# Optimization experiments

Hardware: AMD Instinct MI355X
Metric: run time of the kernel (lower is better)

The kernel has to match this reference:

```python
import jax, jax.numpy as jnp
import numpy as np

# dims
B, N, NF, NEF = 32, 256, 3, 3          # batch, nodes, node feats, edge feats
D, FF, H, L = 768, 3072, 12, 6         # embed, ffn, heads, layers
NA, ND, NE, NS = 512, 512, 512, 512    # vocab sizes (atoms, degrees, edges, spatial)
S = N + 1                              # +1 graph token
HD = D // H
SCALE = HD ** -0.5
EPS = 1e-5


def setup_inputs() -> dict:
    key = jax.random.key(0)
    ki = iter(jax.random.split(key, 64))
    def nrm(shape, std):
        return jax.random.normal(next(ki), shape, jnp.float32) * std
    lin_std = 0.02 / np.sqrt(L)
    inp = {}
    inp['x'] = jax.random.randint(next(ki), (B, N, NF), 0, NA)
    inp['attn_bias'] = jnp.zeros((B, S, S), jnp.float32)
    inp['spatial_pos'] = jax.random.randint(next(ki), (B, N, N), 0, NS)
    inp['attn_edge_type'] = jax.random.randint(next(ki), (B, N, N, NEF), 0, NE)
    inp['in_degree'] = jax.random.randint(next(ki), (B, N), 0, ND)
    inp['out_degree'] = jax.random.randint(next(ki), (B, N), 0, ND)
    # embedding tables (init_params overwrites padding rows with normals, so no zero row)
    inp['atom_emb'] = nrm((NA + 1, D), 0.02)
    inp['in_deg_emb'] = nrm((ND, D), 0.02)
    inp['out_deg_emb'] = nrm((ND, D), 0.02)
    inp['graph_token'] = nrm((1, D), 0.02)
    inp['spatial_emb'] = nrm((NS, H), 0.02)
    inp['edge_emb'] = nrm((NE + 1, H), 0.02)
    inp['virt_dist'] = nrm((1, H), 0.02)
    # stacked per-layer params (torch Linear convention: W is [out,in])
    for nm in ('Wq', 'Wk', 'Wv', 'Wo'):
        inp[nm] = nrm((L, D, D), lin_std)
    for nm in ('bq', 'bk', 'bv', 'bo'):
        inp[nm] = jnp.zeros((L, D), jnp.float32)
    inp['ln1_g'] = jnp.ones((L, D), jnp.float32); inp['ln1_b'] = jnp.zeros((L, D), jnp.float32)
    inp['ln2_g'] = jnp.ones((L, D), jnp.float32); inp['ln2_b'] = jnp.zeros((L, D), jnp.float32)
    inp['W1'] = nrm((L, FF, D), lin_std); inp['b1'] = jnp.zeros((L, FF), jnp.float32)
    inp['W2'] = nrm((L, D, FF), lin_std); inp['b2'] = jnp.zeros((L, D), jnp.float32)
    inp['fin_g'] = jnp.ones((D,), jnp.float32); inp['fin_b'] = jnp.zeros((D,), jnp.float32)
    return inp


def _ln(x, g, b):
    m = x.mean(-1, keepdims=True)
    v = jnp.mean((x - m) ** 2, axis=-1, keepdims=True)
    return (x - m) * jax.lax.rsqrt(v + EPS) * g + b


def _forward(x, attn_bias, spatial_pos, attn_edge_type, in_degree, out_degree, P):
    # --- GraphNodeFeature ---
    nf = P['atom_emb'][jnp.clip(x, 0, NA)].sum(-2)                     # [B,N,D]
    nf = nf + P['in_deg_emb'][jnp.clip(in_degree, 0, ND - 1)]
    nf = nf + P['out_deg_emb'][jnp.clip(out_degree, 0, ND - 1)]
    h = jnp.concatenate([jnp.broadcast_to(P['graph_token'][None], (B, 1, D)), nf], axis=1)  # [B,S,D]
    # --- GraphAttnBias ---
    inner = (P['spatial_emb'][jnp.clip(spatial_pos, 0, NS - 1)]
             + P['edge_emb'][jnp.clip(attn_edge_type, 0, NE)].mean(-2))  # [B,N,N,H]
    gb = jnp.broadcast_to(attn_bias[:, None], (B, H, S, S))
    gb = gb.at[:, :, 1:, 1:].add(jnp.transpose(inner, (0, 3, 1, 2)))
    t = P['virt_dist'].reshape(1, H, 1)
    gb = gb.at[:, :, 1:, 0].add(t)
    gb = gb.at[:, :, 0, :].add(t)
    # key padding mask: node is padded iff first feature index == 0; graph token never padded
    pad = jnp.concatenate([jnp.zeros((B, 1), bool), x[:, :, 0] == 0], axis=1)  # [B,S]
    maskk = pad[:, None, None, :]

    def step(hh, p):
        Wq, bq, Wk, bk, Wv, bv, Wo, bo, g1, bb_g1, W1, bf1, W2, bf2, g2, bb_g2 = p
        # pre-LN self-attention
        z = _ln(hh, g1, bb_g1)
        q = (jnp.einsum('bsi,oi->bso', z, Wq) + bq) * SCALE
        k = jnp.einsum('bsi,oi->bso', z, Wk) + bk
        v = jnp.einsum('bsi,oi->bso', z, Wv) + bv
        q = q.reshape(B, S, H, HD); k = k.reshape(B, S, H, HD); v = v.reshape(B, S, H, HD)
        scores = jnp.einsum('bqhd,bkhd->bhqk', q, k) + gb
        scores = jnp.where(maskk, -jnp.inf, scores)
        a = jax.nn.softmax(scores, axis=-1)
        o = jnp.einsum('bhqk,bkhd->bqhd', a, v).reshape(B, S, D)
        hh = hh + jnp.einsum('bsi,oi->bso', o, Wo) + bo
        # pre-LN FFN
        z = _ln(hh, g2, bb_g2)
        f = jax.nn.gelu(jnp.einsum('bsi,oi->bso', z, W1) + bf1, approximate=False)
        hh = hh + jnp.einsum('bsi,oi->bso', f, W2) + bf2
        return hh, None

    layer_params = (P['Wq'], P['bq'], P['Wk'], P['bk'], P['Wv'], P['bv'], P['Wo'], P['bo'],
                    P['ln1_g'], P['ln1_b'], P['W1'], P['b1'], P['W2'], P['b2'], P['ln2_g'], P['ln2_b'])
    h, _ = jax.lax.scan(step, h, layer_params)
    h = _ln(h, P['fin_g'], P['fin_b'])
    return h  # [B,S,D]


def reference(x, attn_bias, spatial_pos, attn_edge_type, in_degree, out_degree,
              atom_emb, in_deg_emb, out_deg_emb, graph_token, spatial_emb, edge_emb, virt_dist,
              Wq, Wk, Wv, Wo, bq, bk, bv, bo, ln1_g, ln1_b, ln2_g, ln2_b,
              W1, b1, W2, b2, fin_g, fin_b):
    P = dict(atom_emb=atom_emb, in_deg_emb=in_deg_emb, out_deg_emb=out_deg_emb,
             graph_token=graph_token, spatial_emb=spatial_emb, edge_emb=edge_emb, virt_dist=virt_dist,
             Wq=Wq, Wk=Wk, Wv=Wv, Wo=Wo, bq=bq, bk=bk, bv=bv, bo=bo,
             ln1_g=ln1_g, ln1_b=ln1_b, ln2_g=ln2_g, ln2_b=ln2_b,
             W1=W1, b1=b1, W2=W2, b2=b2, fin_g=fin_g, fin_b=fin_b)
    h = _forward(x, attn_bias, spatial_pos, attn_edge_type, in_degree, out_degree, P)
    node_rep = h[:, 1:, :]   # [B,N,D]
    graph_rep = h[:, 0, :]   # [B,D]
    return node_rep, graph_rep
```

## Files before the change

### kernel.cpp

```cpp
#include <hip/hip_runtime.h>
#include <hip/hip_bf16.h>
#include <math.h>

#define B_   32
#define N_   256
#define S_   257
#define D_   768
#define FF_  3072
#define H_   12
#define HD_  64
#define L_   6
#define NA_  512
#define ND_  512
#define NE_  512
#define NS_  512
#define SCALE_ 0.125f
#define EPS_ 1e-5f
#define NEG_BIG_ (-1e30f)

#define DD_  (D_ * D_)
#define FD_  (FF_ * D_)
#define WTOT_ (4 * DD_ + 2 * FD_)
#define QKVN_ 2304

typedef __hip_bfloat16 bf16;
typedef __attribute__((ext_vector_type(8))) short bf16x8;
typedef __attribute__((ext_vector_type(4))) float f32x4;

#define AS1 __attribute__((address_space(1)))
#define AS3 __attribute__((address_space(3)))

static __device__ __forceinline__ int iclamp(int v, int lo, int hi) {
    return v < lo ? lo : (v > hi ? hi : v);
}
static __device__ __forceinline__ float b2f(bf16 v) { return (float)v; }
static __device__ __forceinline__ short f2b(float f) {
    union { bf16 b; short s; } u; u.b = __float2bfloat16(f); return u.s;
}

__global__ __launch_bounds__(256) void embed_kernel(
    const int* __restrict__ x, const int* __restrict__ indeg,
    const int* __restrict__ outdeg, const float* __restrict__ atom_emb,
    const float* __restrict__ ine, const float* __restrict__ oute,
    const float* __restrict__ gtok, float* __restrict__ h)
{
    int row = blockIdx.x;
    int b = row / S_, s = row % S_;
    int t = threadIdx.x;
    float* hr = h + (size_t)row * D_;
    if (s == 0) {
        for (int d = t; d < D_; d += 256) hr[d] = gtok[d];
        return;
    }
    int n = s - 1;
    size_t xb = ((size_t)b * N_ + n) * 3;
    int i0 = iclamp(x[xb + 0], 0, NA_);
    int i1 = iclamp(x[xb + 1], 0, NA_);
    int i2 = iclamp(x[xb + 2], 0, NA_);
    int id = iclamp(indeg[(size_t)b * N_ + n], 0, ND_ - 1);
    int od = iclamp(outdeg[(size_t)b * N_ + n], 0, ND_ - 1);
    const float* a0 = atom_emb + (size_t)i0 * D_;
    const float* a1 = atom_emb + (size_t)i1 * D_;
    const float* a2 = atom_emb + (size_t)i2 * D_;
    const float* pi = ine + (size_t)id * D_;
    const float* po = oute + (size_t)od * D_;
    for (int d = t; d < D_; d += 256)
        hr[d] = a0[d] + a1[d] + a2[d] + pi[d] + po[d];
}

__global__ __launch_bounds__(256) void bias_kernel(
    const int* __restrict__ x, const float* __restrict__ ab,
    const int* __restrict__ sp, const int* __restrict__ et,
    const float* __restrict__ spemb, const float* __restrict__ eemb,
    const float* __restrict__ virt, bf16* __restrict__ bias)
{
    int row = blockIdx.x;
    int b = row / S_, q = row % S_;
    for (int k = threadIdx.x; k < S_; k += 256) {
        float abv = ab[((size_t)b * S_ + q) * S_ + k];
        bool masked = (k >= 1) && (x[((size_t)b * N_ + (k - 1)) * 3] == 0);
        size_t out_base = (size_t)b * H_ * S_ * S_ + (size_t)q * S_ + k;
        if (masked) {
            #pragma unroll
            for (int hh = 0; hh < H_; hh++)
                bias[out_base + (size_t)hh * S_ * S_] = __float2bfloat16(NEG_BIG_);
        } else if (q == 0 || k == 0) {
            #pragma unroll
            for (int hh = 0; hh < H_; hh++)
                bias[out_base + (size_t)hh * S_ * S_] = __float2bfloat16(abv + virt[hh]);
        } else {
            int spv = iclamp(sp[((size_t)b * N_ + (q - 1)) * N_ + (k - 1)], 0, NS_ - 1);
            size_t eb = (((size_t)b * N_ + (q - 1)) * N_ + (k - 1)) * 3;
            int e0 = iclamp(et[eb + 0], 0, NE_);
            int e1 = iclamp(et[eb + 1], 0, NE_);
            int e2 = iclamp(et[eb + 2], 0, NE_);
            #pragma unroll
            for (int hh = 0; hh < H_; hh++) {
                float inner = spemb[spv * H_ + hh]
                    + (eemb[e0 * H_ + hh] + eemb[e1 * H_ + hh] + eemb[e2 * H_ + hh]) * (1.0f / 3.0f);
                bias[out_base + (size_t)hh * S_ * S_] = __float2bfloat16(abv + inner);
            }
        }
    }
}

__global__ __launch_bounds__(256) void cvt_w_kernel(
    const float* __restrict__ Wq, const float* __restrict__ Wk,
    const float* __restrict__ Wv, const float* __restrict__ Wo,
    const float* __restrict__ W1, const float* __restrict__ W2,
    int layer, bf16* __restrict__ dst)
{
    size_t i = ((size_t)blockIdx.x * 256 + threadIdx.x) * 8;
    if (i >= (size_t)WTOT_) return;
    const float* src;
    float sc = 1.f;
    if (i < (size_t)4 * DD_) {
        size_t r = i / DD_;
        const float* base = (r == 0) ? Wq : (r == 1) ? Wk : (r == 2) ? Wv : Wo;
        src = base + (size_t)layer * DD_ + (i - r * DD_);
        if (r == 0) sc = SCALE_;
    } else if (i < (size_t)4 * DD_ + FD_) {
        src = W1 + (size_t)layer * FD_ + (i - (size_t)4 * DD_);
    } else {
        src = W2 + (size_t)layer * FD_ + (i - (size_t)4 * DD_ - FD_);
    }
    float4 a = *(const float4*)src;
    float4 c = *(const float4*)(src + 4);
    *(bf16x8*)((short*)dst + i) =
        (bf16x8){f2b(a.x * sc), f2b(a.y * sc), f2b(a.z * sc), f2b(a.w * sc),
                 f2b(c.x * sc), f2b(c.y * sc), f2b(c.z * sc), f2b(c.w * sc)};
}

__global__ __launch_bounds__(256) void pack_bias_kernel(
    const float* __restrict__ bq, const float* __restrict__ bk,
    const float* __restrict__ bv, int layer, float* __restrict__ bqkv)
{
    int i = blockIdx.x * 256 + threadIdx.x;
    if (i >= QKVN_) return;
    float v;
    if (i < D_)            v = bq[layer * D_ + i] * SCALE_;
    else if (i < 2 * D_)   v = bk[layer * D_ + (i - D_)];
    else                   v = bv[layer * D_ + (i - 2 * D_)];
    bqkv[i] = v;
}

__global__ __launch_bounds__(256) void ln_kernel(
    const float* __restrict__ x, bf16* __restrict__ y,
    const float* __restrict__ g, const float* __restrict__ b)
{
    int row = blockIdx.x;
    int t = threadIdx.x;
    const float* xr = x + (size_t)row * D_;
    bf16* yr = y + (size_t)row * D_;
    float v0 = xr[t], v1 = xr[t + 256], v2 = xr[t + 512];
    __shared__ float rs[256], rq[256];
    rs[t] = v0 + v1 + v2;
    rq[t] = v0 * v0 + v1 * v1 + v2 * v2;
    __syncthreads();
    for (int o = 128; o > 0; o >>= 1) {
        if (t < o) { rs[t] += rs[t + o]; rq[t] += rq[t + o]; }
        __syncthreads();
    }
    float mean = rs[0] * (1.0f / D_);
    float var = fmaxf(rq[0] * (1.0f / D_) - mean * mean, 0.f);
    float inv = rsqrtf(var + EPS_);
    yr[t]       = __float2bfloat16((v0 - mean) * inv * g[t]       + b[t]);
    yr[t + 256] = __float2bfloat16((v1 - mean) * inv * g[t + 256] + b[t + 256]);
    yr[t + 512] = __float2bfloat16((v2 - mean) * inv * g[t + 512] + b[t + 512]);
}

__global__ __launch_bounds__(256) void final_ln_kernel(
    const float* __restrict__ x, const float* __restrict__ g,
    const float* __restrict__ b, float* __restrict__ out)
{
    int row = blockIdx.x;
    int bb = row / S_, s = row % S_;
    int t = threadIdx.x;
    const float* xr = x + (size_t)row * D_;
    float v0 = xr[t], v1 = xr[t + 256], v2 = xr[t + 512];
    __shared__ float rs[256], rq[256];
    rs[t] = v0 + v1 + v2;
    rq[t] = v0 * v0 + v1 * v1 + v2 * v2;
    __syncthreads();
    for (int o = 128; o > 0; o >>= 1) {
        if (t < o) { rs[t] += rs[t + o]; rq[t] += rq[t + o]; }
        __syncthreads();
    }
    float mean = rs[0] * (1.0f / D_);
    float var = fmaxf(rq[0] * (1.0f / D_) - mean * mean, 0.f);
    float inv = rsqrtf(var + EPS_);
    float* dst = (s == 0) ? out + (size_t)B_ * N_ * D_ + (size_t)bb * D_
                          : out + ((size_t)bb * N_ + (s - 1)) * D_;
    dst[t]       = (v0 - mean) * inv * g[t]       + b[t];
    dst[t + 256] = (v1 - mean) * inv * g[t + 256] + b[t + 256];
    dst[t + 512] = (v2 - mean) * inv * g[t + 512] + b[t + 512];
}

template <typename TC, int MODE>
__global__ __launch_bounds__(256) void mgemm(
    const bf16* __restrict__ A, const bf16* __restrict__ W,
    const float* __restrict__ bias, const float* __restrict__ res,
    TC* __restrict__ C, int M, int N, int K, int gx)
{
    __shared__ short As[2][128 * 32];
    __shared__ short Ws[2][128 * 32];
    AS3 short* AsL = (AS3 short*)&As[0][0];
    AS3 short* WsL = (AS3 short*)&Ws[0][0];
    const int t = threadIdx.x;
    const int lane = t & 63;
    const int w = t >> 6;
    const int wm = w & 1, wn = w >> 1;
    const int quad = lane >> 4;
    const int col = lane & 15;

    const int nwg = gridDim.x;
    const int orig = blockIdx.x;
    const int q8 = nwg >> 3, r8 = nwg & 7;
    const int xcd = orig & 7, li = orig >> 3;
    const int wgid = (xcd < r8 ? xcd * (q8 + 1) : r8 * (q8 + 1) + (xcd - r8) * q8) + li;
    const int block_m = (wgid % gx) * 128;
    const int block_n = (wgid / gx) * 128;

    const int lrow = lane >> 2;
    const int lcol = (lane & 3) * 8;

    auto stage = [&](int buf, int k0) {
        #pragma unroll
        for (int ss = 0; ss < 2; ss++) {
            int seg = w * 2 + ss;
            int row = seg * 16 + lrow;
            const bf16* ga = A + (size_t)(block_m + row) * K + k0 + lcol;
            __builtin_amdgcn_global_load_lds((const AS1 void*)ga,
                (AS3 void*)(AsL + buf * (128 * 32) + seg * 512), 16, 0, 0);
            const bf16* gw = W + (size_t)(block_n + row) * K + k0 + lcol;
            __builtin_amdgcn_global_load_lds((const AS1 void*)gw,
                (AS3 void*)(WsL + buf * (128 * 32) + seg * 512), 16, 0, 0);
        }
    };

    f32x4 acc[4][4];
    #pragma unroll
    for (int i = 0; i < 4; i++)
        #pragma unroll
        for (int j = 0; j < 4; j++)
            acc[i][j] = (f32x4){0.f, 0.f, 0.f, 0.f};

    const int nt = K >> 5;
    stage(0, 0);
    __syncthreads();
    int cur = 0;
    for (int tt = 0; tt < nt; tt++) {
        if (tt + 1 < nt) stage(cur ^ 1, (tt + 1) << 5);
        bf16x8 af[4], bfr[4];
        #pragma unroll
        for (int mt = 0; mt < 4; mt++)
            af[mt] = *(const bf16x8*)&As[cur][(wm * 64 + mt * 16 + col) * 32 + quad * 8];
        #pragma unroll
        for (int ntt = 0; ntt < 4; ntt++)
            bfr[ntt] = *(const bf16x8*)&Ws[cur][(wn * 64 + ntt * 16 + col) * 32 + quad * 8];
        #pragma unroll
        for (int mt = 0; mt < 4; mt++)
            #pragma unroll
            for (int ntt = 0; ntt < 4; ntt++)
                acc[mt][ntt] = __builtin_amdgcn_mfma_f32_16x16x32_bf16(
                    af[mt], bfr[ntt], acc[mt][ntt], 0, 0, 0);
        __syncthreads();
        cur ^= 1;
    }

    #pragma unroll
    for (int mt = 0; mt < 4; mt++) {
        #pragma unroll
        for (int ntt = 0; ntt < 4; ntt++) {
            int gn = block_n + wn * 64 + ntt * 16 + col;
            float bn = bias[gn];
            #pragma unroll
            for (int r = 0; r < 4; r++) {
                int gm = block_m + wm * 64 + mt * 16 + quad * 4 + r;
                if (gm < M) {
                    float val = acc[mt][ntt][r] + bn;
                    if (MODE == 2) val = 0.5f * val * (1.0f + erff(val * 0.70710678118654752f));
                    if (MODE == 3) val += res[(size_t)gm * N + gn];
                    C[(size_t)gm * N + gn] = (TC)val;
                }
            }
        }
    }
}

__global__ __launch_bounds__(256) void attn_mfma(
    const bf16* __restrict__ qkv, const bf16* __restrict__ bias,
    bf16* __restrict__ ob)
{
    const bf16* qb = qkv;
    const bf16* kb = qkv + D_;
    const bf16* vb = qkv + 2 * D_;
    __shared__ short Ks[64 * 72];
    __shared__ short Vt[64 * 72];
    __shared__ short Ps[4][16 * 72];

    const int t = threadIdx.x;
    const int lane = t & 63;
    const int wq = t >> 6;
    const int quad = lane >> 4;
    const int col = lane & 15;
    const int bh = blockIdx.y;
    const int hh = bh % H_;
    const int b = bh / H_;
    const int q0 = blockIdx.x * 64;

    bf16x8 qf[2];
    {
        int qrow = q0 + wq * 16 + col;
        #pragma unroll
        for (int kk = 0; kk < 2; kk++) {
            bf16x8 v = (bf16x8){0, 0, 0, 0, 0, 0, 0, 0};
            if (qrow < S_)
                v = *(const bf16x8*)(qb + ((size_t)(b * S_ + qrow)) * QKVN_ + hh * HD_ + kk * 32 + quad * 8);
            qf[kk] = v;
        }
    }

    f32x4 o_acc[4];
    #pragma unroll
    for (int nt = 0; nt < 4; nt++) o_acc[nt] = (f32x4){0.f, 0.f, 0.f, 0.f};
    float m_run[4], l_run[4];
    #pragma unroll
    for (int r = 0; r < 4; r++) { m_run[r] = NEG_BIG_; l_run[r] = 0.f; }

    for (int kc = 0; kc < 5; kc++) {
        const int kbase = kc * 64;
        #pragma unroll
        for (int ss = 0; ss < 2; ss++) {
            int s = t + ss * 256;
            int row = s >> 3, dg = (s & 7) * 8;
            int gk = kbase + row;
            bf16x8 v = (bf16x8){0, 0, 0, 0, 0, 0, 0, 0};
            if (gk < S_)
                v = *(const bf16x8*)(kb + ((size_t)(b * S_ + gk)) * QKVN_ + hh * HD_ + dg);
            *(bf16x8*)&Ks[row * 72 + dg] = v;
        }
        {
            int d = wq * 16 + col;
            const bf16* vcol = vb + ((size_t)(b * S_)) * QKVN_ + hh * HD_ + d;
            #pragma unroll
            for (int ss = 0; ss < 8; ss++) {
                int kp = ss * 4 + quad;
                int gk = kbase + kp * 2;
                short v0 = (gk     < S_) ? *(const short*)(vcol + (size_t)gk * QKVN_)       : (short)0;
                short v1 = (gk + 1 < S_) ? *(const short*)(vcol + (size_t)(gk + 1) * QKVN_) : (short)0;
                unsigned pk = ((unsigned)(unsigned short)v0) |
                              ((unsigned)(unsigned short)v1 << 16);
                *(unsigned*)&Vt[d * 72 + kp * 2] = pk;
            }
        }
        __syncthreads();

        f32x4 s_acc[4];
        #pragma unroll
        for (int nt = 0; nt < 4; nt++) s_acc[nt] = (f32x4){0.f, 0.f, 0.f, 0.f};
        #pragma unroll
        for (int nt = 0; nt < 4; nt++) {
            #pragma unroll
            for (int kk = 0; kk < 2; kk++) {
                bf16x8 kfrag = *(const bf16x8*)&Ks[(nt * 16 + col) * 72 + kk * 32 + quad * 8];
                s_acc[nt] = __builtin_amdgcn_mfma_f32_16x16x32_bf16(qf[kk], kfrag, s_acc[nt], 0, 0, 0);
            }
        }

        const int qrow_base = q0 + wq * 16 + quad * 4;
        #pragma unroll
        for (int nt = 0; nt < 4; nt++) {
            int kglob = kbase + nt * 16 + col;
            #pragma unroll
            for (int r = 0; r < 4; r++) {
                int q = qrow_base + r;
                float sv = s_acc[nt][r];
                if (kglob >= S_)       sv = NEG_BIG_;
                else if (q < S_)       sv += b2f(bias[((size_t)bh * S_ + q) * S_ + kglob]);
                s_acc[nt][r] = sv;
            }
        }

        float alpha[4];
        #pragma unroll
        for (int r = 0; r < 4; r++) {
            float mx = fmaxf(fmaxf(s_acc[0][r], s_acc[1][r]),
                             fmaxf(s_acc[2][r], s_acc[3][r]));
            #pragma unroll
            for (int off = 8; off; off >>= 1) mx = fmaxf(mx, __shfl_xor(mx, off));
            float m_new = fmaxf(m_run[r], mx);
            alpha[r] = __expf(m_run[r] - m_new);
            m_run[r] = m_new;
            float ps = 0.f;
            #pragma unroll
            for (int nt = 0; nt < 4; nt++) {
                float p = __expf(s_acc[nt][r] - m_new);
                s_acc[nt][r] = p;
                ps += p;
            }
            #pragma unroll
            for (int off = 8; off; off >>= 1) ps += __shfl_xor(ps, off);
            l_run[r] = l_run[r] * alpha[r] + ps;
        }

        #pragma unroll
        for (int nt = 0; nt < 4; nt++)
            #pragma unroll
            for (int r = 0; r < 4; r++)
                Ps[wq][(quad * 4 + r) * 72 + nt * 16 + col] = f2b(s_acc[nt][r]);
        #pragma unroll
        for (int nt = 0; nt < 4; nt++)
            #pragma unroll
            for (int r = 0; r < 4; r++)
                o_acc[nt][r] *= alpha[r];

        bf16x8 pf[2];
        pf[0] = *(const bf16x8*)&Ps[wq][col * 72 + quad * 8];
        pf[1] = *(const bf16x8*)&Ps[wq][col * 72 + 32 + quad * 8];
        #pragma unroll
        for (int nt = 0; nt < 4; nt++) {
            #pragma unroll
            for (int kk = 0; kk < 2; kk++) {
                bf16x8 vfrag = *(const bf16x8*)&Vt[(nt * 16 + col) * 72 + kk * 32 + quad * 8];
                o_acc[nt] = __builtin_amdgcn_mfma_f32_16x16x32_bf16(pf[kk], vfrag, o_acc[nt], 0, 0, 0);
            }
        }
        __syncthreads();
    }

    const int qrow_base = q0 + wq * 16 + quad * 4;
    #pragma unroll
    for (int r = 0; r < 4; r++) {
        int q = qrow_base + r;
        if (q >= S_) continue;
        float invl = 1.0f / l_run[r];
        bf16* orow = ob + ((size_t)(b * S_ + q)) * D_ + hh * HD_;
        #pragma unroll
        for (int nt = 0; nt < 4; nt++)
            orow[nt * 16 + col] = __float2bfloat16(o_acc[nt][r] * invl);
    }
}

extern "C" void kernel_launch(void* const* d_in, const int* in_sizes, int n_in,
                              void* d_out, int out_size, void* d_ws, size_t ws_size,
                              hipStream_t stream)
{
    const int*   x         = (const int*)d_in[0];
    const float* attn_bias = (const float*)d_in[1];
    const int*   spatial   = (const int*)d_in[2];
    const int*   edget     = (const int*)d_in[3];
    const int*   indeg     = (const int*)d_in[4];
    const int*   outdeg    = (const int*)d_in[5];
    const float* atom_emb  = (const float*)d_in[6];
    const float* ine       = (const float*)d_in[7];
    const float* oute      = (const float*)d_in[8];
    const float* gtok      = (const float*)d_in[9];
    const float* spemb     = (const float*)d_in[10];
    const float* eemb      = (const float*)d_in[11];
    const float* virt      = (const float*)d_in[12];
    const float* Wq        = (const float*)d_in[13];
    const float* Wk        = (const float*)d_in[14];
    const float* Wv        = (const float*)d_in[15];
    const float* Wo        = (const float*)d_in[16];
    const float* bq        = (const float*)d_in[17];
    const float* bk        = (const float*)d_in[18];
    const float* bvv       = (const float*)d_in[19];
    const float* bo        = (const float*)d_in[20];
    const float* ln1g      = (const float*)d_in[21];
    const float* ln1b      = (const float*)d_in[22];
    const float* ln2g      = (const float*)d_in[23];
    const float* ln2b      = (const float*)d_in[24];
    const float* W1        = (const float*)d_in[25];
    const float* b1        = (const float*)d_in[26];
    const float* W2        = (const float*)d_in[27];
    const float* b2        = (const float*)d_in[28];
    const float* fing      = (const float*)d_in[29];
    const float* finb      = (const float*)d_in[30];

    const int M = B_ * S_;
    char* wsp = (char*)d_ws;
    size_t off = 0;
    auto alloc = [&](size_t bytes) -> void* {
        void* p = (void*)(wsp + off);
        off += (bytes + 255) & ~(size_t)255;
        return p;
    };
    float* h    = (float*)alloc((size_t)M * D_ * 4);
    bf16*  z    = (bf16*)alloc((size_t)M * D_ * 2);
    bf16*  qkv  = (bf16*)alloc((size_t)M * FF_ * 2);
    bf16*  bias = (bf16*)alloc((size_t)B_ * H_ * S_ * S_ * 2);
    bf16*  wbf  = (bf16*)alloc((size_t)WTOT_ * 2);
    float* bqkv = (float*)alloc((size_t)QKVN_ * 4);
    bf16* fbuf = qkv;
    bf16* obuf = z;

    embed_kernel<<<M, 256, 0, stream>>>(x, indeg, outdeg, atom_emb, ine, oute, gtok, h);
    bias_kernel<<<M, 256, 0, stream>>>(x, attn_bias, spatial, edget, spemb, eemb, virt, bias);

    const int gx = (M + 127) / 128;
    const int nQKV = gx * (QKVN_ / 128);
    const int nD   = gx * (D_ / 128);
    const int nF   = gx * (FF_ / 128);
    dim3 gA(5, B_ * H_);
    const int cvtBlocks = WTOT_ / 2048;

    for (int l = 0; l < L_; l++) {
        cvt_w_kernel<<<cvtBlocks, 256, 0, stream>>>(Wq, Wk, Wv, Wo, W1, W2, l, wbf);
        pack_bias_kernel<<<9, 256, 0, stream>>>(bq, bk, bvv, l, bqkv);
        ln_kernel<<<M, 256, 0, stream>>>(h, z, ln1g + l * D_, ln1b + l * D_);
        mgemm<bf16, 0><<<nQKV, 256, 0, stream>>>(z, wbf, bqkv, nullptr, qkv, M, QKVN_, D_, gx);
        attn_mfma<<<gA, 256, 0, stream>>>(qkv, bias, obuf);
        mgemm<float, 3><<<nD, 256, 0, stream>>>(obuf, wbf + 3 * DD_, bo + l * D_, h, h, M, D_, D_, gx);
        ln_kernel<<<M, 256, 0, stream>>>(h, z, ln2g + l * D_, ln2b + l * D_);
        mgemm<bf16, 2><<<nF, 256, 0, stream>>>(z, wbf + 4 * DD_, b1 + l * FF_, nullptr, fbuf, M, FF_, D_, gx);
        mgemm<float, 3><<<nD, 256, 0, stream>>>(fbuf, wbf + 4 * DD_ + FD_, b2 + l * D_, h, h, M, D_, FF_, gx);
    }
    final_ln_kernel<<<M, 256, 0, stream>>>(h, fing, finb, (float*)d_out);
}
```

Before: 2.562 ms.

## Replace GEMM with 256-row, 8-wave tiles using swizzled LDS and split-phase pipelining

Replaces the 128x128, 4-wave, K=32 GEMM with a 256xBN tile (BN=256 for the QKV and FFN1 GEMMs, 128 for the two D-output GEMMs) run by 8 waves with K=64 stages. LDS rows are XOR-swizzled to avoid bank conflicts. The k-loop is split into four phases with explicit vmcnt waits and raw barriers, so A and B chunk loads for the next stages overlap with MFMA work. The goal is more operand reuse per byte loaded and fewer stalls. In exchange, the larger tiles mean fewer workgroups and possibly lower occupancy, and the hand-written waitcnt counts are fragile.

```diff
diff --git a/kernel.cpp b/kernel.cpp
--- a/kernel.cpp
+++ b/kernel.cpp
@@ -30,6 +30,13 @@
 #define AS1 __attribute__((address_space(1)))
 #define AS3 __attribute__((address_space(3)))
 
+#define BAR()  asm volatile("s_barrier" ::: "memory")
+#define VM0()  asm volatile("s_waitcnt vmcnt(0)" ::: "memory")
+#define VM2()  asm volatile("s_waitcnt vmcnt(2)" ::: "memory")
+#define VM4()  asm volatile("s_waitcnt vmcnt(4)" ::: "memory")
+#define VM6()  asm volatile("s_waitcnt vmcnt(6)" ::: "memory")
+#define VM8()  asm volatile("s_waitcnt vmcnt(8)" ::: "memory")
+
 static __device__ __forceinline__ int iclamp(int v, int lo, int hi) {
     return v < lo ? lo : (v > hi ? hi : v);
 }
@@ -196,89 +203,171 @@
     dst[t + 512] = (v2 - mean) * inv * g[t + 512] + b[t + 512];
 }
 
-template <typename TC, int MODE>
-__global__ __launch_bounds__(256) void mgemm(
+template <int BN, int MODE, typename TC>
+__global__ __launch_bounds__(512, 1) void mgemm2(
     const bf16* __restrict__ A, const bf16* __restrict__ W,
     const float* __restrict__ bias, const float* __restrict__ res,
     TC* __restrict__ C, int M, int N, int K, int gx)
 {
-    __shared__ short As[2][128 * 32];
-    __shared__ short Ws[2][128 * 32];
-    AS3 short* AsL = (AS3 short*)&As[0][0];
-    AS3 short* WsL = (AS3 short*)&Ws[0][0];
+    constexpr int NTW = BN / 64;
+    constexpr int WN  = BN / 4;
+    constexpr int BCH = BN / 64;
+    constexpr int BSZ = BN * 64;
+
+    __shared__ short Asm[2][256 * 64];
+    __shared__ short Bsm[2][BSZ];
+    AS3 short* AsL = (AS3 short*)&Asm[0][0];
+    AS3 short* BsL = (AS3 short*)&Bsm[0][0];
+
     const int t = threadIdx.x;
     const int lane = t & 63;
-    const int w = t >> 6;
-    const int wm = w & 1, wn = w >> 1;
+    const int wid = t >> 6;
+    const int wm = wid >> 2;
+    const int wn = wid & 3;
     const int quad = lane >> 4;
-    const int col = lane & 15;
+    const int col16 = lane & 15;
+    const int r7 = col16 & 7;
 
     const int nwg = gridDim.x;
     const int orig = blockIdx.x;
     const int q8 = nwg >> 3, r8 = nwg & 7;
     const int xcd = orig & 7, li = orig >> 3;
     const int wgid = (xcd < r8 ? xcd * (q8 + 1) : r8 * (q8 + 1) + (xcd - r8) * q8) + li;
-    const int block_m = (wgid % gx) * 128;
-    const int block_n = (wgid / gx) * 128;
-
-    const int lrow = lane >> 2;
-    const int lcol = (lane & 3) * 8;
-
-    auto stage = [&](int buf, int k0) {
-        #pragma unroll
-        for (int ss = 0; ss < 2; ss++) {
-            int seg = w * 2 + ss;
-            int row = seg * 16 + lrow;
-            const bf16* ga = A + (size_t)(block_m + row) * K + k0 + lcol;
-            __builtin_amdgcn_global_load_lds((const AS1 void*)ga,
-                (AS3 void*)(AsL + buf * (128 * 32) + seg * 512), 16, 0, 0);
-            const bf16* gw = W + (size_t)(block_n + row) * K + k0 + lcol;
-            __builtin_amdgcn_global_load_lds((const AS1 void*)gw,
-                (AS3 void*)(WsL + buf * (128 * 32) + seg * 512), 16, 0, 0);
-        }
+    const int block_m = (wgid % gx) * 256;
+    const int block_n = (wgid / gx) * BN;
+
+    const int lgb = ((lane & 7) ^ (lane >> 3)) * 8;
+
+    auto stA = [&](int db, int T, int chunk) {
+        int row = chunk * 64 + wid * 8 + (lane >> 3);
+        const bf16* src = A + (size_t)(block_m + row) * K + T * 64 + lgb;
+        __builtin_amdgcn_global_load_lds((const AS1 void*)src,
+            (AS3 void*)(AsL + db * 16384 + (chunk * 512 + wid * 64) * 8), 16, 0, 0);
     };
-
-    f32x4 acc[4][4];
+    auto stB = [&](int db, int T, int chunk) {
+        int row = chunk * 64 + wid * 8 + (lane >> 3);
+        const bf16* src = W + (size_t)(block_n + row) * K + T * 64 + lgb;
+        __builtin_amdgcn_global_load_lds((const AS1 void*)src,
+            (AS3 void*)(BsL + db * BSZ + (chunk * 512 + wid * 64) * 8), 16, 0, 0);
+    };
+
+    f32x4 acc[8][NTW];
     #pragma unroll
-    for (int i = 0; i < 4; i++)
-        #pragma unroll
-        for (int j = 0; j < 4; j++)
+    for (int i = 0; i < 8; i++)
+        #pragma unroll
+        for (int j = 0; j < NTW; j++)
             acc[i][j] = (f32x4){0.f, 0.f, 0.f, 0.f};
 
-    const int nt = K >> 5;
-    stage(0, 0);
-    __syncthreads();
-    int cur = 0;
-    for (int tt = 0; tt < nt; tt++) {
-        if (tt + 1 < nt) stage(cur ^ 1, (tt + 1) << 5);
-        bf16x8 af[4], bfr[4];
-        #pragma unroll
-        for (int mt = 0; mt < 4; mt++)
-            af[mt] = *(const bf16x8*)&As[cur][(wm * 64 + mt * 16 + col) * 32 + quad * 8];
-        #pragma unroll
-        for (int ntt = 0; ntt < 4; ntt++)
-            bfr[ntt] = *(const bf16x8*)&Ws[cur][(wn * 64 + ntt * 16 + col) * 32 + quad * 8];
-        #pragma unroll
-        for (int mt = 0; mt < 4; mt++)
-            #pragma unroll
-            for (int ntt = 0; ntt < 4; ntt++)
-                acc[mt][ntt] = __builtin_amdgcn_mfma_f32_16x16x32_bf16(
-                    af[mt], bfr[ntt], acc[mt][ntt], 0, 0, 0);
-        __syncthreads();
-        cur ^= 1;
-    }
-
+    const int nt = K >> 6;
+
+    stA(0, 0, 0); stA(0, 0, 1); stA(0, 0, 2); stA(0, 0, 3);
     #pragma unroll
-    for (int mt = 0; mt < 4; mt++) {
-        #pragma unroll
-        for (int ntt = 0; ntt < 4; ntt++) {
-            int gn = block_n + wn * 64 + ntt * 16 + col;
+    for (int ch = 0; ch < BCH; ch++) stB(0, 0, ch);
+    #pragma unroll
+    for (int ch = 0; ch < BCH; ch++) stB(1, 1, ch);
+    stA(1, 1, 0); stA(1, 1, 2);
+    if constexpr (BCH == 4) VM6(); else VM4();
+    BAR();
+
+    for (int g = 0; g < nt; ++g) {
+        const int c = g & 1;
+
+        if (g + 1 < nt) { stA(c ^ 1, g + 1, 1); stA(c ^ 1, g + 1, 3); }
+        bf16x8 bfr[NTW][2];
+        #pragma unroll
+        for (int j = 0; j < NTW; j++)
+            #pragma unroll
+            for (int ks = 0; ks < 2; ks++)
+                bfr[j][ks] = *(const bf16x8*)&Bsm[c][(wn * WN + j * 16 + col16) * 64 + ((ks * 4 + quad) ^ r7) * 8];
+        {
+            bf16x8 a0[2], a1[2];
+            #pragma unroll
+            for (int ks = 0; ks < 2; ks++) {
+                a0[ks] = *(const bf16x8*)&Asm[c][(wm * 128 + 0 * 16 + col16) * 64 + ((ks * 4 + quad) ^ r7) * 8];
+                a1[ks] = *(const bf16x8*)&Asm[c][(wm * 128 + 1 * 16 + col16) * 64 + ((ks * 4 + quad) ^ r7) * 8];
+            }
+            #pragma unroll
+            for (int j = 0; j < NTW; j++)
+                #pragma unroll
+                for (int ks = 0; ks < 2; ks++) {
+                    acc[0][j] = __builtin_amdgcn_mfma_f32_16x16x32_bf16(a0[ks], bfr[j][ks], acc[0][j], 0, 0, 0);
+                    acc[1][j] = __builtin_amdgcn_mfma_f32_16x16x32_bf16(a1[ks], bfr[j][ks], acc[1][j], 0, 0, 0);
+                }
+        }
+        BAR();
+
+        if (g + 2 < nt) { stB(c, g + 2, 0); stB(c, g + 2, 1); }
+        {
+            bf16x8 a0[2], a1[2];
+            #pragma unroll
+            for (int ks = 0; ks < 2; ks++) {
+                a0[ks] = *(const bf16x8*)&Asm[c][(wm * 128 + 2 * 16 + col16) * 64 + ((ks * 4 + quad) ^ r7) * 8];
+                a1[ks] = *(const bf16x8*)&Asm[c][(wm * 128 + 3 * 16 + col16) * 64 + ((ks * 4 + quad) ^ r7) * 8];
+            }
+            #pragma unroll
+            for (int j = 0; j < NTW; j++)
+                #pragma unroll
+                for (int ks = 0; ks < 2; ks++) {
+                    acc[2][j] = __builtin_amdgcn_mfma_f32_16x16x32_bf16(a0[ks], bfr[j][ks], acc[2][j], 0, 0, 0);
+                    acc[3][j] = __builtin_amdgcn_mfma_f32_16x16x32_bf16(a1[ks], bfr[j][ks], acc[3][j], 0, 0, 0);
+                }
+        }
+        if (g == nt - 1) VM0();
+        else { if constexpr (BCH == 4) VM8(); else VM6(); }
+        BAR();
+
+        if constexpr (BCH == 4) {
+            if (g + 2 < nt) { stB(c, g + 2, 2); stB(c, g + 2, 3); }
+        }
+        {
+            bf16x8 a0[2], a1[2];
+            #pragma unroll
+            for (int ks = 0; ks < 2; ks++) {
+                a0[ks] = *(const bf16x8*)&Asm[c][(wm * 128 + 4 * 16 + col16) * 64 + ((ks * 4 + quad) ^ r7) * 8];
+                a1[ks] = *(const bf16x8*)&Asm[c][(wm * 128 + 5 * 16 + col16) * 64 + ((ks * 4 + quad) ^ r7) * 8];
+            }
+            #pragma unroll
+            for (int j = 0; j < NTW; j++)
+                #pragma unroll
+                for (int ks = 0; ks < 2; ks++) {
+                    acc[4][j] = __builtin_amdgcn_mfma_f32_16x16x32_bf16(a0[ks], bfr[j][ks], acc[4][j], 0, 0, 0);
+                    acc[5][j] = __builtin_amdgcn_mfma_f32_16x16x32_bf16(a1[ks], bfr[j][ks], acc[5][j], 0, 0, 0);
+                }
+        }
+        BAR();
+
+        if (g + 2 < nt) { stA(c, g + 2, 0); stA(c, g + 2, 2); }
+        {
+            bf16x8 a0[2], a1[2];
+            #pragma unroll
+            for (int ks = 0; ks < 2; ks++) {
+                a0[ks] = *(const bf16x8*)&Asm[c][(wm * 128 + 6 * 16 + col16) * 64 + ((ks * 4 + quad) ^ r7) * 8];
+                a1[ks] = *(const bf16x8*)&Asm[c][(wm * 128 + 7 * 16 + col16) * 64 + ((ks * 4 + quad) ^ r7) * 8];
+            }
+            #pragma unroll
+            for (int j = 0; j < NTW; j++)
+                #pragma unroll
+                for (int ks = 0; ks < 2; ks++) {
+                    acc[6][j] = __builtin_amdgcn_mfma_f32_16x16x32_bf16(a0[ks], bfr[j][ks], acc[6][j], 0, 0, 0);
+                    acc[7][j] = __builtin_amdgcn_mfma_f32_16x16x32_bf16(a1[ks], bfr[j][ks], acc[7][j], 0, 0, 0);
+                }
+        }
+        if (g == nt - 2) { VM2(); }
+        else if (g < nt - 2) { if constexpr (BCH == 4) VM8(); else VM6(); }
+        BAR();
+    }
+
+    #pragma unroll
+    for (int mt = 0; mt < 8; mt++) {
+        #pragma unroll
+        for (int j = 0; j < NTW; j++) {
+            int gn = block_n + wn * WN + j * 16 + col16;
             float bn = bias[gn];
             #pragma unroll
             for (int r = 0; r < 4; r++) {
-                int gm = block_m + wm * 64 + mt * 16 + quad * 4 + r;
+                int gm = block_m + wm * 128 + mt * 16 + quad * 4 + r;
                 if (gm < M) {
-                    float val = acc[mt][ntt][r] + bn;
+                    float val = acc[mt][j][r] + bn;
                     if (MODE == 2) val = 0.5f * val * (1.0f + erff(val * 0.70710678118654752f));
                     if (MODE == 3) val += res[(size_t)gm * N + gn];
                     C[(size_t)gm * N + gn] = (TC)val;
@@ -498,10 +587,10 @@
     embed_kernel<<<M, 256, 0, stream>>>(x, indeg, outdeg, atom_emb, ine, oute, gtok, h);
     bias_kernel<<<M, 256, 0, stream>>>(x, attn_bias, spatial, edget, spemb, eemb, virt, bias);
 
-    const int gx = (M + 127) / 128;
-    const int nQKV = gx * (QKVN_ / 128);
+    const int gx = (M + 255) / 256;
+    const int nQKV = gx * (QKVN_ / 256);
     const int nD   = gx * (D_ / 128);
-    const int nF   = gx * (FF_ / 128);
+    const int nF   = gx * (FF_ / 256);
     dim3 gA(5, B_ * H_);
     const int cvtBlocks = WTOT_ / 2048;
 
@@ -509,12 +598,12 @@
         cvt_w_kernel<<<cvtBlocks, 256, 0, stream>>>(Wq, Wk, Wv, Wo, W1, W2, l, wbf);
         pack_bias_kernel<<<9, 256, 0, stream>>>(bq, bk, bvv, l, bqkv);
         ln_kernel<<<M, 256, 0, stream>>>(h, z, ln1g + l * D_, ln1b + l * D_);
-        mgemm<bf16, 0><<<nQKV, 256, 0, stream>>>(z, wbf, bqkv, nullptr, qkv, M, QKVN_, D_, gx);
+        mgemm2<256, 0, bf16><<<nQKV, 512, 0, stream>>>(z, wbf, bqkv, nullptr, qkv, M, QKVN_, D_, gx);
         attn_mfma<<<gA, 256, 0, stream>>>(qkv, bias, obuf);
-        mgemm<float, 3><<<nD, 256, 0, stream>>>(obuf, wbf + 3 * DD_, bo + l * D_, h, h, M, D_, D_, gx);
+        mgemm2<128, 3, float><<<nD, 512, 0, stream>>>(obuf, wbf + 3 * DD_, bo + l * D_, h, h, M, D_, D_, gx);
         ln_kernel<<<M, 256, 0, stream>>>(h, z, ln2g + l * D_, ln2b + l * D_);
-        mgemm<bf16, 2><<<nF, 256, 0, stream>>>(z, wbf + 4 * DD_, b1 + l * FF_, nullptr, fbuf, M, FF_, D_, gx);
-        mgemm<float, 3><<<nD, 256, 0, stream>>>(fbuf, wbf + 4 * DD_ + FD_, b2 + l * D_, h, h, M, D_, FF_, gx);
+        mgemm2<256, 2, bf16><<<nF, 512, 0, stream>>>(z, wbf + 4 * DD_, b1 + l * FF_, nullptr, fbuf, M, FF_, D_, gx);
+        mgemm2<128, 3, float><<<nD, 512, 0, stream>>>(fbuf, wbf + 4 * DD_ + FD_, b2 + l * D_, h, h, M, D_, FF_, gx);
     }
     final_ln_kernel<<<M, 256, 0, stream>>>(h, fing, finb, (float*)d_out);
 }
```

Result: slower. 2.936 ms (+14.6%).
